# Optimization experiments

Measured on AMD Instinct MI355X. Metric: run time of the kernel, lower is better.

The kernel has to match this reference:

```python
import jax, jax.numpy as jnp
import numpy as np

EMBED_DIM = 768
HIDDEN = 768


def setup_inputs() -> dict:
    key = jax.random.key(0)
    k1, k2, k3, k4 = jax.random.split(key, 4)
    doc_embed = jax.random.normal(k1, (32, 1024, EMBED_DIM), dtype=jnp.float32)
    query_embed = jax.random.normal(k2, (32, 128, EMBED_DIM), dtype=jnp.float32)
    # nn.Linear params: weight [H, E], bias [H]
    bound = 1.0 / np.sqrt(EMBED_DIM)
    W = jax.random.uniform(k3, (HIDDEN, EMBED_DIM), minval=-bound, maxval=bound, dtype=jnp.float32)
    b = jax.random.uniform(k4, (HIDDEN,), minval=-bound, maxval=bound, dtype=jnp.float32)
    return {"doc_embed": doc_embed, "query_embed": query_embed, "W": W, "b": b}


def reference(doc_embed, query_embed, W, b):
    # shared linear projection + ReLU
    doc_o = jax.nn.relu(jnp.einsum('bde,he->bdh', doc_embed, W) + b)    # [B, Ld, H]
    query_o = jax.nn.relu(jnp.einsum('bqe,he->bqh', query_embed, W) + b)  # [B, Lq, H]
    # unscaled cross-attention scores over query positions
    scores = jnp.einsum('bdh,bqh->bdq', doc_o, query_o)  # [B, Ld, Lq]
    attn = jax.nn.softmax(scores, axis=-1)
    out = jnp.einsum('bdq,bqe->bde', attn, query_embed)  # [B, Ld, E]
    return out
```

## Files before the change

kernel.cpp:

```cpp
#include <hip/hip_runtime.h>

typedef _Float16 f16x8 __attribute__((ext_vector_type(8)));
typedef float f32x4 __attribute__((ext_vector_type(4)));

#define EMB 768
#define LQ 128
#define LD 1024
#define NB 32

typedef const __attribute__((address_space(1))) char gas_char;
typedef __attribute__((address_space(3))) char las_char;

__device__ __forceinline__ void gload16(const void* g, void* l) {
    __builtin_amdgcn_global_load_lds((gas_char*)g, (las_char*)l, 16, 0, 0);
}

#define SWZ(row, ch) ((row) * 64 + ((((ch) ^ ((row) & 7))) * 8))

__device__ __forceinline__ void stage_tile(const _Float16* g, _Float16* l, int wave, int lane) {
#pragma unroll
    for (int i = 0; i < 4; ++i) {
        const int idx = i * 256 + wave * 64 + lane;
        const int row = idx >> 3, ch = idx & 7;
        const int lch = ch ^ (row & 7);
        gload16(g + (size_t)row * EMB + lch * 8, l + (size_t)(i * 256 + wave * 64) * 8);
    }
}

__global__ void cvt8_kernel(const float* __restrict__ in, _Float16* __restrict__ out, int n8) {
    int i = blockIdx.x * 256 + threadIdx.x;
    if (i >= n8) return;
    const float4 a = ((const float4*)in)[2 * i];
    const float4 b = ((const float4*)in)[2 * i + 1];
    f16x8 o;
    o[0] = (_Float16)a.x; o[1] = (_Float16)a.y; o[2] = (_Float16)a.z; o[3] = (_Float16)a.w;
    o[4] = (_Float16)b.x; o[5] = (_Float16)b.y; o[6] = (_Float16)b.z; o[7] = (_Float16)b.w;
    ((f16x8*)out)[i] = o;
}

__global__ void make_vt_kernel(const float* __restrict__ Q, _Float16* __restrict__ VT) {
    int i = blockIdx.x * 256 + threadIdx.x;
    if (i >= NB * EMB * LQ) return;
    int q = i % LQ;
    int e = (i / LQ) % EMB;
    int b = i / (LQ * EMB);
    VT[i] = (_Float16)Q[((size_t)b * LQ + q) * EMB + e];
}

__global__ __launch_bounds__(256) void proj128_kernel(
    const _Float16* __restrict__ A, const _Float16* __restrict__ B,
    const float* __restrict__ bias, _Float16* __restrict__ OUT) {
    __shared__ __align__(16) _Float16 smem[32768];
    const int tid = threadIdx.x, wave = tid >> 6, lane = tid & 63;
    const int wr = wave >> 1, wc = wave & 1;
    const int lr = lane & 15, lkg = lane >> 4;
    const int row0 = blockIdx.x * 128, col0 = blockIdx.y * 128;
    const _Float16* ga = A + (size_t)row0 * EMB;
    const _Float16* gb = B + (size_t)col0 * EMB;

    f32x4 acc[4][4];
#pragma unroll
    for (int m = 0; m < 4; ++m)
#pragma unroll
        for (int n = 0; n < 4; ++n) acc[m][n] = (f32x4){0.f, 0.f, 0.f, 0.f};

    stage_tile(ga, smem, wave, lane);
    stage_tile(gb, smem + 8192, wave, lane);
    int cur = 0;
    for (int it = 0; it < 12; ++it) {
        __syncthreads();
        if (it < 11) {
            stage_tile(ga + (it + 1) * 64, smem + (cur ^ 1) * 16384, wave, lane);
            stage_tile(gb + (it + 1) * 64, smem + (cur ^ 1) * 16384 + 8192, wave, lane);
        }
        const _Float16* sA = smem + cur * 16384;
        const _Float16* sB = smem + cur * 16384 + 8192;
#pragma unroll
        for (int kk = 0; kk < 2; ++kk) {
            const int ch = kk * 4 + lkg;
            f16x8 af[4], bf[4];
#pragma unroll
            for (int m = 0; m < 4; ++m)
                af[m] = *(const f16x8*)(sA + SWZ(wr * 64 + m * 16 + lr, ch));
#pragma unroll
            for (int n = 0; n < 4; ++n)
                bf[n] = *(const f16x8*)(sB + SWZ(wc * 64 + n * 16 + lr, ch));
#pragma unroll
            for (int m = 0; m < 4; ++m)
#pragma unroll
                for (int n = 0; n < 4; ++n)
                    acc[m][n] = __builtin_amdgcn_mfma_f32_16x16x32_f16(af[m], bf[n], acc[m][n], 0, 0, 0);
        }
        cur ^= 1;
    }
    const int crow = lkg * 4;
#pragma unroll
    for (int n = 0; n < 4; ++n) {
        const int gc = col0 + wc * 64 + n * 16 + lr;
        const float bv = bias[gc];
#pragma unroll
        for (int m = 0; m < 4; ++m) {
            const size_t gr = row0 + wr * 64 + m * 16 + crow;
#pragma unroll
            for (int r = 0; r < 4; ++r) {
                float v = acc[m][n][r] + bv;
                OUT[(gr + r) * EMB + gc] = (_Float16)(v > 0.f ? v : 0.f);
            }
        }
    }
}

__global__ __launch_bounds__(256) void attn128_kernel(
    const _Float16* __restrict__ Do, const _Float16* __restrict__ Qo,
    const _Float16* __restrict__ VT, float* __restrict__ OUT) {
    __shared__ __align__(16) _Float16 smem[32768];
    const int tid = threadIdx.x, wave = tid >> 6, lane = tid & 63;
    const int lr = lane & 15, lkg = lane >> 4;
    const int b = blockIdx.x, dblk = blockIdx.y;
    const _Float16* gd = Do + ((size_t)b * LD + dblk * 128) * EMB;
    const _Float16* gq = Qo + (size_t)b * LQ * EMB;

    f32x4 s[2][8];
#pragma unroll
    for (int m = 0; m < 2; ++m)
#pragma unroll
        for (int n = 0; n < 8; ++n) s[m][n] = (f32x4){0.f, 0.f, 0.f, 0.f};

    stage_tile(gd, smem, wave, lane);
    stage_tile(gq, smem + 8192, wave, lane);
    int cur = 0;
    for (int it = 0; it < 12; ++it) {
        __syncthreads();
        if (it < 11) {
            stage_tile(gd + (it + 1) * 64, smem + (cur ^ 1) * 16384, wave, lane);
            stage_tile(gq + (it + 1) * 64, smem + (cur ^ 1) * 16384 + 8192, wave, lane);
        }
        const _Float16* sD = smem + cur * 16384;
        const _Float16* sQ = smem + cur * 16384 + 8192;
#pragma unroll
        for (int kk = 0; kk < 2; ++kk) {
            const int ch = kk * 4 + lkg;
            f16x8 am[2];
#pragma unroll
            for (int m = 0; m < 2; ++m)
                am[m] = *(const f16x8*)(sD + SWZ(wave * 32 + m * 16 + lr, ch));
#pragma unroll
            for (int n = 0; n < 8; ++n) {
                const f16x8 bq = *(const f16x8*)(sQ + SWZ(n * 16 + lr, ch));
#pragma unroll
                for (int m = 0; m < 2; ++m)
                    s[m][n] = __builtin_amdgcn_mfma_f32_16x16x32_f16(am[m], bq, s[m][n], 0, 0, 0);
            }
        }
        cur ^= 1;
    }
    __syncthreads();

    _Float16 (*P)[136] = (_Float16 (*)[136])smem;
    const int crow = lkg * 4;
#pragma unroll
    for (int m = 0; m < 2; ++m) {
#pragma unroll
        for (int r = 0; r < 4; ++r) {
            float mx = -1e30f;
#pragma unroll
            for (int n = 0; n < 8; ++n) mx = fmaxf(mx, s[m][n][r]);
#pragma unroll
            for (int off = 1; off < 16; off <<= 1) mx = fmaxf(mx, __shfl_xor(mx, off));
            float p[8], sum = 0.f;
#pragma unroll
            for (int n = 0; n < 8; ++n) { p[n] = __expf(s[m][n][r] - mx); sum += p[n]; }
#pragma unroll
            for (int off = 1; off < 16; off <<= 1) sum += __shfl_xor(sum, off);
            const float inv = 1.f / sum;
            const int row = wave * 32 + m * 16 + crow + r;
#pragma unroll
            for (int n = 0; n < 8; ++n) P[row][n * 16 + lr] = (_Float16)(p[n] * inv);
        }
    }
    __syncthreads();

    const _Float16* vtb = VT + (size_t)b * EMB * LQ;
#pragma unroll 1
    for (int nc = 0; nc < 6; ++nc) {
        f32x4 o[2][8];
#pragma unroll
        for (int m = 0; m < 2; ++m)
#pragma unroll
            for (int t = 0; t < 8; ++t) o[m][t] = (f32x4){0.f, 0.f, 0.f, 0.f};
#pragma unroll
        for (int ks = 0; ks < 4; ++ks) {
            f16x8 am[2];
#pragma unroll
            for (int m = 0; m < 2; ++m)
                am[m] = *(const f16x8*)(&P[wave * 32 + m * 16 + lr][ks * 32 + lkg * 8]);
#pragma unroll
            for (int t = 0; t < 8; ++t) {
                const f16x8 bv = *(const f16x8*)(vtb + (size_t)(nc * 128 + t * 16 + lr) * LQ + ks * 32 + lkg * 8);
#pragma unroll
                for (int m = 0; m < 2; ++m)
                    o[m][t] = __builtin_amdgcn_mfma_f32_16x16x32_f16(am[m], bv, o[m][t], 0, 0, 0);
            }
        }
#pragma unroll
        for (int t = 0; t < 8; ++t) {
#pragma unroll
            for (int m = 0; m < 2; ++m) {
                const size_t gr = (size_t)b * LD + dblk * 128 + wave * 32 + m * 16 + crow;
                const int e = nc * 128 + t * 16 + lr;
#pragma unroll
                for (int r = 0; r < 4; ++r)
                    OUT[(gr + r) * EMB + e] = o[m][t][r];
            }
        }
    }
}

extern "C" void kernel_launch(void* const* d_in, const int* in_sizes, int n_in,
                              void* d_out, int out_size, void* d_ws, size_t ws_size,
                              hipStream_t stream) {
    const float* doc   = (const float*)d_in[0];
    const float* query = (const float*)d_in[1];
    const float* W     = (const float*)d_in[2];
    const float* bias  = (const float*)d_in[3];
    float* out = (float*)d_out;

    const size_t nW  = (size_t)EMB * EMB;
    const size_t nVT = (size_t)NB * EMB * LQ;
    const size_t nQo = (size_t)NB * LQ * EMB;
    const size_t nDo = (size_t)NB * LD * EMB;
    const size_t need = (nW + nVT + nQo + nDo) * sizeof(_Float16);
    if (ws_size < need) return;

    _Float16* W16 = (_Float16*)d_ws;
    _Float16* VT  = W16 + nW;
    _Float16* Qo  = VT + nVT;
    _Float16* Do  = Qo + nQo;

    _Float16* doc16 = (_Float16*)d_out;
    _Float16* q16   = doc16 + nDo;

    cvt8_kernel<<<(int)(nDo / 8 / 256), 256, 0, stream>>>(doc, doc16, (int)(nDo / 8));
    cvt8_kernel<<<(int)(nQo / 8 / 256), 256, 0, stream>>>(query, q16, (int)(nQo / 8));
    cvt8_kernel<<<(int)(nW / 8 / 256), 256, 0, stream>>>(W, W16, (int)(nW / 8));
    make_vt_kernel<<<(int)(nVT / 256), 256, 0, stream>>>(query, VT);

    proj128_kernel<<<dim3(NB * LQ / 128, EMB / 128), 256, 0, stream>>>(q16, W16, bias, Qo);
    proj128_kernel<<<dim3(NB * LD / 128, EMB / 128), 256, 0, stream>>>(doc16, W16, bias, Do);
    attn128_kernel<<<dim3(NB, LD / 128), 256, 0, stream>>>(Do, Qo, VT, out);
}
```

Before: 160.1 us.

## Merge projections into one 256x256 GEMM with triple-buffered LDS; shrink attention tile

The two projection launches become a single 512-thread GEMM over the concatenated doc and query rows, which relies on q16 following doc16 and Qo following Do in memory. It uses 256x256 output tiles, a 3-stage global_load_lds pipeline with explicit waitcnt and barrier scheduling, setprio around the MFMA blocks, and an XCD-aware block remap. The attention kernel moves to 64-row doc tiles with a remapped 1D grid to raise block count and occupancy. The larger tile and the hand-written barrier scheduling are meant to cut global traffic and launch overhead, at the risk of register pressure and fragile synchronization.

```diff
diff --git a/kernel.cpp b/kernel.cpp
--- a/kernel.cpp
+++ b/kernel.cpp
@@ -16,16 +16,7 @@
 }
 
 #define SWZ(row, ch) ((row) * 64 + ((((ch) ^ ((row) & 7))) * 8))
-
-__device__ __forceinline__ void stage_tile(const _Float16* g, _Float16* l, int wave, int lane) {
-#pragma unroll
-    for (int i = 0; i < 4; ++i) {
-        const int idx = i * 256 + wave * 64 + lane;
-        const int row = idx >> 3, ch = idx & 7;
-        const int lch = ch ^ (row & 7);
-        gload16(g + (size_t)row * EMB + lch * 8, l + (size_t)(i * 256 + wave * 64) * 8);
-    }
-}
+#define SWZ32(row, c) ((row) * 32 + ((((c) ^ ((row) & 3) ^ (((row) >> 2) & 3))) * 8))
 
 __global__ void cvt8_kernel(const float* __restrict__ in, _Float16* __restrict__ out, int n8) {
     int i = blockIdx.x * 256 + threadIdx.x;
@@ -47,109 +38,161 @@
     VT[i] = (_Float16)Q[((size_t)b * LQ + q) * EMB + e];
 }
 
-__global__ __launch_bounds__(256) void proj128_kernel(
+__global__ __launch_bounds__(512, 2) void proj256_kernel(
     const _Float16* __restrict__ A, const _Float16* __restrict__ B,
-    const float* __restrict__ bias, _Float16* __restrict__ OUT) {
-    __shared__ __align__(16) _Float16 smem[32768];
+    const float* __restrict__ bias, _Float16* __restrict__ OUT, int nrowblk) {
+    extern __shared__ _Float16 smem[];
     const int tid = threadIdx.x, wave = tid >> 6, lane = tid & 63;
-    const int wr = wave >> 1, wc = wave & 1;
     const int lr = lane & 15, lkg = lane >> 4;
-    const int row0 = blockIdx.x * 128, col0 = blockIdx.y * 128;
-    const _Float16* ga = A + (size_t)row0 * EMB;
-    const _Float16* gb = B + (size_t)col0 * EMB;
-
-    f32x4 acc[4][4];
-#pragma unroll
-    for (int m = 0; m < 4; ++m)
+    const int wr = wave >> 2, wc = wave & 3;
+
+    const int nwg = nrowblk * 3, cpx = nwg >> 3;
+    const int bid = blockIdx.x;
+    const int swz = (bid & 7) * cpx + (bid >> 3);
+    const int rowblk = swz / 3, colblk = swz % 3;
+    const int row0 = rowblk * 256, col0 = colblk * 256;
+
+    const _Float16* gA = A + (size_t)row0 * EMB;
+    const _Float16* gB = B + (size_t)col0 * EMB;
+
+    const int sr0 = tid >> 2, sc = tid & 3;
+    const int sig = (sr0 & 3) ^ ((sr0 >> 2) & 3);
+    const int scs = (sc ^ sig) * 8;
+    const _Float16* srcA0 = gA + (size_t)sr0 * EMB + scs;
+    const _Float16* srcA1 = gA + (size_t)(sr0 + 128) * EMB + scs;
+    const _Float16* srcB0 = gB + (size_t)sr0 * EMB + scs;
+    const _Float16* srcB1 = gB + (size_t)(sr0 + 128) * EMB + scs;
+
+#define STAGE_A(kt, bufi) { _Float16* d = smem + (bufi) * 16384 + wave * 512; \
+        gload16(srcA0 + (kt) * 32, d); gload16(srcA1 + (kt) * 32, d + 4096); }
+#define STAGE_B(kt, bufi) { _Float16* d = smem + (bufi) * 16384 + 8192 + wave * 512; \
+        gload16(srcB0 + (kt) * 32, d); gload16(srcB1 + (kt) * 32, d + 4096); }
+
+    f32x4 acc[8][4];
+#pragma unroll
+    for (int m = 0; m < 8; ++m)
 #pragma unroll
         for (int n = 0; n < 4; ++n) acc[m][n] = (f32x4){0.f, 0.f, 0.f, 0.f};
 
-    stage_tile(ga, smem, wave, lane);
-    stage_tile(gb, smem + 8192, wave, lane);
+    const int rdoff = ((lkg ^ (lr & 3) ^ ((lr >> 2) & 3)) * 8);
+
+    STAGE_A(0, 0); STAGE_B(0, 0); STAGE_A(1, 1); STAGE_B(1, 1);
+    asm volatile("s_waitcnt vmcnt(4)" ::: "memory");
+    __builtin_amdgcn_s_barrier();
+
+    int bi = 0;
+    for (int j = 0; j < 24; ++j) {
+        const _Float16* bufA = smem + bi * 16384;
+        const _Float16* bufB = bufA + 8192;
+        int nb = bi + 2; if (nb >= 3) nb -= 3;
+        f16x8 bf[4], af[4];
+#pragma unroll
+        for (int n = 0; n < 4; ++n)
+            bf[n] = *(const f16x8*)(bufB + (wc * 64 + n * 16 + lr) * 32 + rdoff);
+#pragma unroll
+        for (int m = 0; m < 4; ++m)
+            af[m] = *(const f16x8*)(bufA + (wr * 128 + m * 16 + lr) * 32 + rdoff);
+        if (j + 2 < 24) { STAGE_A(j + 2, nb); }
+        __builtin_amdgcn_s_barrier();
+        asm volatile("s_waitcnt lgkmcnt(0)" ::: "memory");
+        __builtin_amdgcn_sched_barrier(0);
+        __builtin_amdgcn_s_setprio(1);
+#pragma unroll
+        for (int m = 0; m < 4; ++m)
+#pragma unroll
+            for (int n = 0; n < 4; ++n)
+                acc[m][n] = __builtin_amdgcn_mfma_f32_16x16x32_f16(af[m], bf[n], acc[m][n], 0, 0, 0);
+        __builtin_amdgcn_s_setprio(0);
+        __builtin_amdgcn_s_barrier();
+#pragma unroll
+        for (int m = 0; m < 4; ++m)
+            af[m] = *(const f16x8*)(bufA + (wr * 128 + (m + 4) * 16 + lr) * 32 + rdoff);
+        if (j + 2 < 24) { STAGE_B(j + 2, nb); }
+        if (j + 3 < 24) { asm volatile("s_waitcnt vmcnt(4)" ::: "memory"); }
+        else            { asm volatile("s_waitcnt vmcnt(0)" ::: "memory"); }
+        __builtin_amdgcn_s_barrier();
+        asm volatile("s_waitcnt lgkmcnt(0)" ::: "memory");
+        __builtin_amdgcn_sched_barrier(0);
+        __builtin_amdgcn_s_setprio(1);
+#pragma unroll
+        for (int m = 0; m < 4; ++m)
+#pragma unroll
+            for (int n = 0; n < 4; ++n)
+                acc[m + 4][n] = __builtin_amdgcn_mfma_f32_16x16x32_f16(af[m], bf[n], acc[m + 4][n], 0, 0, 0);
+        __builtin_amdgcn_s_setprio(0);
+        __builtin_amdgcn_s_barrier();
+        bi = (bi == 2) ? 0 : bi + 1;
+    }
+
+    const int crow = lkg * 4;
+#pragma unroll
+    for (int n = 0; n < 4; ++n) {
+        const int gc = col0 + wc * 64 + n * 16 + lr;
+        const float bv = bias[gc];
+#pragma unroll
+        for (int m = 0; m < 8; ++m) {
+            const size_t gr = (size_t)row0 + wr * 128 + m * 16 + crow;
+#pragma unroll
+            for (int r = 0; r < 4; ++r) {
+                float v = acc[m][n][r] + bv;
+                OUT[(gr + r) * EMB + gc] = (_Float16)(v > 0.f ? v : 0.f);
+            }
+        }
+    }
+#undef STAGE_A
+#undef STAGE_B
+}
+
+__global__ __launch_bounds__(256) void attn64_kernel(
+    const _Float16* __restrict__ Do, const _Float16* __restrict__ Qo,
+    const _Float16* __restrict__ VT, float* __restrict__ OUT) {
+    __shared__ __align__(16) _Float16 smem[24576];
+    const int tid = threadIdx.x, wave = tid >> 6, lane = tid & 63;
+    const int lr = lane & 15, lkg = lane >> 4;
+
+    const int l = blockIdx.x;
+    const int x = l & 7, i = l >> 3;
+    const int b = x * 4 + (i >> 4), dblk = i & 15;
+
+    const _Float16* gd = Do + ((size_t)b * LD + dblk * 64) * EMB;
+    const _Float16* gq = Qo + (size_t)b * LQ * EMB;
+
+    f32x4 s[8];
+#pragma unroll
+    for (int n = 0; n < 8; ++n) s[n] = (f32x4){0.f, 0.f, 0.f, 0.f};
+
+#define STAGE_D(g, base) { \
+    _Float16* lb = (base); \
+    { int idx = tid;       int row = idx >> 3, ch = idx & 7; int lch = ch ^ (row & 7); \
+      gload16((g) + (size_t)row * EMB + lch * 8, lb + (size_t)(wave * 64) * 8); } \
+    { int idx = 256 + tid; int row = idx >> 3, ch = idx & 7; int lch = ch ^ (row & 7); \
+      gload16((g) + (size_t)row * EMB + lch * 8, lb + (size_t)(256 + wave * 64) * 8); } }
+#define STAGE_Q(g, base) { \
+    _Float16* lb = (base); \
+    _Pragma("unroll") \
+    for (int it2 = 0; it2 < 4; ++it2) { \
+      int idx = it2 * 256 + tid; int row = idx >> 3, ch = idx & 7; int lch = ch ^ (row & 7); \
+      gload16((g) + (size_t)row * EMB + lch * 8, lb + (size_t)(it2 * 256 + wave * 64) * 8); } }
+
+    STAGE_D(gd, smem);
+    STAGE_Q(gq, smem + 4096);
     int cur = 0;
     for (int it = 0; it < 12; ++it) {
         __syncthreads();
         if (it < 11) {
-            stage_tile(ga + (it + 1) * 64, smem + (cur ^ 1) * 16384, wave, lane);
-            stage_tile(gb + (it + 1) * 64, smem + (cur ^ 1) * 16384 + 8192, wave, lane);
-        }
-        const _Float16* sA = smem + cur * 16384;
-        const _Float16* sB = smem + cur * 16384 + 8192;
+            STAGE_D(gd + (it + 1) * 64, smem + (cur ^ 1) * 12288);
+            STAGE_Q(gq + (it + 1) * 64, smem + (cur ^ 1) * 12288 + 4096);
+        }
+        const _Float16* sD = smem + cur * 12288;
+        const _Float16* sQ = sD + 4096;
 #pragma unroll
         for (int kk = 0; kk < 2; ++kk) {
             const int ch = kk * 4 + lkg;
-            f16x8 af[4], bf[4];
-#pragma unroll
-            for (int m = 0; m < 4; ++m)
-                af[m] = *(const f16x8*)(sA + SWZ(wr * 64 + m * 16 + lr, ch));
-#pragma unroll
-            for (int n = 0; n < 4; ++n)
-                bf[n] = *(const f16x8*)(sB + SWZ(wc * 64 + n * 16 + lr, ch));
-#pragma unroll
-            for (int m = 0; m < 4; ++m)
-#pragma unroll
-                for (int n = 0; n < 4; ++n)
-                    acc[m][n] = __builtin_amdgcn_mfma_f32_16x16x32_f16(af[m], bf[n], acc[m][n], 0, 0, 0);
-        }
-        cur ^= 1;
-    }
-    const int crow = lkg * 4;
-#pragma unroll
-    for (int n = 0; n < 4; ++n) {
-        const int gc = col0 + wc * 64 + n * 16 + lr;
-        const float bv = bias[gc];
-#pragma unroll
-        for (int m = 0; m < 4; ++m) {
-            const size_t gr = row0 + wr * 64 + m * 16 + crow;
-#pragma unroll
-            for (int r = 0; r < 4; ++r) {
-                float v = acc[m][n][r] + bv;
-                OUT[(gr + r) * EMB + gc] = (_Float16)(v > 0.f ? v : 0.f);
-            }
-        }
-    }
-}
-
-__global__ __launch_bounds__(256) void attn128_kernel(
-    const _Float16* __restrict__ Do, const _Float16* __restrict__ Qo,
-    const _Float16* __restrict__ VT, float* __restrict__ OUT) {
-    __shared__ __align__(16) _Float16 smem[32768];
-    const int tid = threadIdx.x, wave = tid >> 6, lane = tid & 63;
-    const int lr = lane & 15, lkg = lane >> 4;
-    const int b = blockIdx.x, dblk = blockIdx.y;
-    const _Float16* gd = Do + ((size_t)b * LD + dblk * 128) * EMB;
-    const _Float16* gq = Qo + (size_t)b * LQ * EMB;
-
-    f32x4 s[2][8];
-#pragma unroll
-    for (int m = 0; m < 2; ++m)
-#pragma unroll
-        for (int n = 0; n < 8; ++n) s[m][n] = (f32x4){0.f, 0.f, 0.f, 0.f};
-
-    stage_tile(gd, smem, wave, lane);
-    stage_tile(gq, smem + 8192, wave, lane);
-    int cur = 0;
-    for (int it = 0; it < 12; ++it) {
-        __syncthreads();
-        if (it < 11) {
-            stage_tile(gd + (it + 1) * 64, smem + (cur ^ 1) * 16384, wave, lane);
-            stage_tile(gq + (it + 1) * 64, smem + (cur ^ 1) * 16384 + 8192, wave, lane);
-        }
-        const _Float16* sD = smem + cur * 16384;
-        const _Float16* sQ = smem + cur * 16384 + 8192;
-#pragma unroll
-        for (int kk = 0; kk < 2; ++kk) {
-            const int ch = kk * 4 + lkg;
-            f16x8 am[2];
-#pragma unroll
-            for (int m = 0; m < 2; ++m)
-                am[m] = *(const f16x8*)(sD + SWZ(wave * 32 + m * 16 + lr, ch));
+            const f16x8 af = *(const f16x8*)(sD + SWZ(wave * 16 + lr, ch));
 #pragma unroll
             for (int n = 0; n < 8; ++n) {
                 const f16x8 bq = *(const f16x8*)(sQ + SWZ(n * 16 + lr, ch));
-#pragma unroll
-                for (int m = 0; m < 2; ++m)
-                    s[m][n] = __builtin_amdgcn_mfma_f32_16x16x32_f16(am[m], bq, s[m][n], 0, 0, 0);
+                s[n] = __builtin_amdgcn_mfma_f32_16x16x32_f16(af, bq, s[n], 0, 0, 0);
             }
         }
         cur ^= 1;
@@ -159,61 +202,50 @@
     _Float16 (*P)[136] = (_Float16 (*)[136])smem;
     const int crow = lkg * 4;
 #pragma unroll
-    for (int m = 0; m < 2; ++m) {
-#pragma unroll
-        for (int r = 0; r < 4; ++r) {
-            float mx = -1e30f;
-#pragma unroll
-            for (int n = 0; n < 8; ++n) mx = fmaxf(mx, s[m][n][r]);
-#pragma unroll
-            for (int off = 1; off < 16; off <<= 1) mx = fmaxf(mx, __shfl_xor(mx, off));
-            float p[8], sum = 0.f;
-#pragma unroll
-            for (int n = 0; n < 8; ++n) { p[n] = __expf(s[m][n][r] - mx); sum += p[n]; }
-#pragma unroll
-            for (int off = 1; off < 16; off <<= 1) sum += __shfl_xor(sum, off);
-            const float inv = 1.f / sum;
-            const int row = wave * 32 + m * 16 + crow + r;
-#pragma unroll
-            for (int n = 0; n < 8; ++n) P[row][n * 16 + lr] = (_Float16)(p[n] * inv);
-        }
+    for (int r = 0; r < 4; ++r) {
+        float mx = -1e30f;
+#pragma unroll
+        for (int n = 0; n < 8; ++n) mx = fmaxf(mx, s[n][r]);
+#pragma unroll
+        for (int off = 1; off < 16; off <<= 1) mx = fmaxf(mx, __shfl_xor(mx, off));
+        float p[8], sum = 0.f;
+#pragma unroll
+        for (int n = 0; n < 8; ++n) { p[n] = __expf(s[n][r] - mx); sum += p[n]; }
+#pragma unroll
+        for (int off = 1; off < 16; off <<= 1) sum += __shfl_xor(sum, off);
+        const float inv = 1.f / sum;
+        const int row = wave * 16 + crow + r;
+#pragma unroll
+        for (int n = 0; n < 8; ++n) P[row][n * 16 + lr] = (_Float16)(p[n] * inv);
     }
     __syncthreads();
 
     const _Float16* vtb = VT + (size_t)b * EMB * LQ;
+    const size_t dbase = (size_t)b * LD + dblk * 64 + wave * 16 + crow;
 #pragma unroll 1
     for (int nc = 0; nc < 6; ++nc) {
-        f32x4 o[2][8];
-#pragma unroll
-        for (int m = 0; m < 2; ++m)
-#pragma unroll
-            for (int t = 0; t < 8; ++t) o[m][t] = (f32x4){0.f, 0.f, 0.f, 0.f};
+        f32x4 o[8];
+#pragma unroll
+        for (int t = 0; t < 8; ++t) o[t] = (f32x4){0.f, 0.f, 0.f, 0.f};
 #pragma unroll
         for (int ks = 0; ks < 4; ++ks) {
-            f16x8 am[2];
-#pragma unroll
-            for (int m = 0; m < 2; ++m)
-                am[m] = *(const f16x8*)(&P[wave * 32 + m * 16 + lr][ks * 32 + lkg * 8]);
+            const f16x8 am = *(const f16x8*)(&P[wave * 16 + lr][ks * 32 + lkg * 8]);
 #pragma unroll
             for (int t = 0; t < 8; ++t) {
                 const f16x8 bv = *(const f16x8*)(vtb + (size_t)(nc * 128 + t * 16 + lr) * LQ + ks * 32 + lkg * 8);
-#pragma unroll
-                for (int m = 0; m < 2; ++m)
-                    o[m][t] = __builtin_amdgcn_mfma_f32_16x16x32_f16(am[m], bv, o[m][t], 0, 0, 0);
+                o[t] = __builtin_amdgcn_mfma_f32_16x16x32_f16(am, bv, o[t], 0, 0, 0);
             }
         }
 #pragma unroll
         for (int t = 0; t < 8; ++t) {
-#pragma unroll
-            for (int m = 0; m < 2; ++m) {
-                const size_t gr = (size_t)b * LD + dblk * 128 + wave * 32 + m * 16 + crow;
-                const int e = nc * 128 + t * 16 + lr;
-#pragma unroll
-                for (int r = 0; r < 4; ++r)
-                    OUT[(gr + r) * EMB + e] = o[m][t][r];
-            }
-        }
-    }
+            const int e = nc * 128 + t * 16 + lr;
+#pragma unroll
+            for (int r = 0; r < 4; ++r)
+                OUT[(dbase + r) * EMB + e] = o[t][r];
+        }
+    }
+#undef STAGE_D
+#undef STAGE_Q
 }
 
 extern "C" void kernel_launch(void* const* d_in, const int* in_sizes, int n_in,
@@ -227,15 +259,15 @@
 
     const size_t nW  = (size_t)EMB * EMB;
     const size_t nVT = (size_t)NB * EMB * LQ;
+    const size_t nDo = (size_t)NB * LD * EMB;
     const size_t nQo = (size_t)NB * LQ * EMB;
-    const size_t nDo = (size_t)NB * LD * EMB;
-    const size_t need = (nW + nVT + nQo + nDo) * sizeof(_Float16);
+    const size_t need = (nW + nVT + nDo + nQo) * sizeof(_Float16);
     if (ws_size < need) return;
 
     _Float16* W16 = (_Float16*)d_ws;
     _Float16* VT  = W16 + nW;
-    _Float16* Qo  = VT + nVT;
-    _Float16* Do  = Qo + nQo;
+    _Float16* Do  = VT + nVT;
+    _Float16* Qo  = Do + nDo;
 
     _Float16* doc16 = (_Float16*)d_out;
     _Float16* q16   = doc16 + nDo;
@@ -245,7 +277,10 @@
     cvt8_kernel<<<(int)(nW / 8 / 256), 256, 0, stream>>>(W, W16, (int)(nW / 8));
     make_vt_kernel<<<(int)(nVT / 256), 256, 0, stream>>>(query, VT);
 
-    proj128_kernel<<<dim3(NB * LQ / 128, EMB / 128), 256, 0, stream>>>(q16, W16, bias, Qo);
-    proj128_kernel<<<dim3(NB * LD / 128, EMB / 128), 256, 0, stream>>>(doc16, W16, bias, Do);
-    attn128_kernel<<<dim3(NB, LD / 128), 256, 0, stream>>>(Do, Qo, VT, out);
-}
+    const int nrowblk = (int)((nDo + nQo) / EMB / 256);
+    hipFuncSetAttribute(reinterpret_cast<const void*>(&proj256_kernel),
+                        hipFuncAttributeMaxDynamicSharedMemorySize, 98304);
+    proj256_kernel<<<dim3(nrowblk * 3), 512, 98304, stream>>>(doc16, W16, bias, Do, nrowblk);
+
+    attn64_kernel<<<dim3(NB * 16), 256, 0, stream>>>(Do, Qo, VT, out);
+}
```

New measurement: 169.0 us. 5.6% more time.

## Fuse doc projection, scores, softmax and PV into one kernel

Applied to the files above, without the earlier changes.

Removes the separate fp16 conversion of doc, the doc projection GEMM, and the Do intermediate buffer. A new fused kernel loads fp32 doc rows straight into registers as fp16 A-fragments. It projects them chunk by chunk against double-buffered W tiles in LDS, applies bias and ReLU, and accumulates the scores against Qo read from global. Softmax and PV follow in the same kernel, which cuts global traffic and launches. The cost is 64-row blocks (512 blocks) with heavy register use, W being restreamed by every block, and Qo and VT loaded directly from global without LDS staging.

```diff
diff --git a/kernel.cpp b/kernel.cpp
--- a/kernel.cpp
+++ b/kernel.cpp
@@ -16,16 +16,6 @@
 }
 
 #define SWZ(row, ch) ((row) * 64 + ((((ch) ^ ((row) & 7))) * 8))
-
-__device__ __forceinline__ void stage_tile(const _Float16* g, _Float16* l, int wave, int lane) {
-#pragma unroll
-    for (int i = 0; i < 4; ++i) {
-        const int idx = i * 256 + wave * 64 + lane;
-        const int row = idx >> 3, ch = idx & 7;
-        const int lch = ch ^ (row & 7);
-        gload16(g + (size_t)row * EMB + lch * 8, l + (size_t)(i * 256 + wave * 64) * 8);
-    }
-}
 
 __global__ void cvt8_kernel(const float* __restrict__ in, _Float16* __restrict__ out, int n8) {
     int i = blockIdx.x * 256 + threadIdx.x;
@@ -45,6 +35,16 @@
     int e = (i / LQ) % EMB;
     int b = i / (LQ * EMB);
     VT[i] = (_Float16)Q[((size_t)b * LQ + q) * EMB + e];
+}
+
+__device__ __forceinline__ void stage_tile(const _Float16* g, _Float16* l, int wave, int lane) {
+#pragma unroll
+    for (int i = 0; i < 4; ++i) {
+        const int idx = i * 256 + wave * 64 + lane;
+        const int row = idx >> 3, ch = idx & 7;
+        const int lch = ch ^ (row & 7);
+        gload16(g + (size_t)row * EMB + lch * 8, l + (size_t)(i * 256 + wave * 64) * 8);
+    }
 }
 
 __global__ __launch_bounds__(256) void proj128_kernel(
@@ -110,108 +110,135 @@
     }
 }
 
-__global__ __launch_bounds__(256) void attn128_kernel(
-    const _Float16* __restrict__ Do, const _Float16* __restrict__ Qo,
+__device__ __forceinline__ void stage_w(const _Float16* __restrict__ W16,
+                                        _Float16* sWbuf, int t, int tid) {
+    const int hc = t / 12, kt = t - hc * 12;
+    const _Float16* gsrc = W16 + (size_t)hc * 128 * EMB + kt * 64;
+#pragma unroll
+    for (int ii = 0; ii < 4; ++ii) {
+        const int idx = ii * 256 + tid;
+        const int row = idx >> 3, ch = idx & 7;
+        gload16(gsrc + (size_t)row * EMB + ((ch ^ (row & 7)) * 8), sWbuf + (size_t)idx * 8);
+    }
+}
+
+__global__ __launch_bounds__(256, 2) void fused_kernel(
+    const float* __restrict__ doc, const _Float16* __restrict__ W16,
+    const float* __restrict__ bias, const _Float16* __restrict__ Qo,
     const _Float16* __restrict__ VT, float* __restrict__ OUT) {
-    __shared__ __align__(16) _Float16 smem[32768];
+    __shared__ __align__(16) _Float16 sW[2 * 8192];
+    __shared__ __align__(16) _Float16 doC[4][16][136];
+
     const int tid = threadIdx.x, wave = tid >> 6, lane = tid & 63;
     const int lr = lane & 15, lkg = lane >> 4;
-    const int b = blockIdx.x, dblk = blockIdx.y;
-    const _Float16* gd = Do + ((size_t)b * LD + dblk * 128) * EMB;
-    const _Float16* gq = Qo + (size_t)b * LQ * EMB;
-
-    f32x4 s[2][8];
-#pragma unroll
-    for (int m = 0; m < 2; ++m)
-#pragma unroll
-        for (int n = 0; n < 8; ++n) s[m][n] = (f32x4){0.f, 0.f, 0.f, 0.f};
-
-    stage_tile(gd, smem, wave, lane);
-    stage_tile(gq, smem + 8192, wave, lane);
-    int cur = 0;
-    for (int it = 0; it < 12; ++it) {
-        __syncthreads();
-        if (it < 11) {
-            stage_tile(gd + (it + 1) * 64, smem + (cur ^ 1) * 16384, wave, lane);
-            stage_tile(gq + (it + 1) * 64, smem + (cur ^ 1) * 16384 + 8192, wave, lane);
-        }
-        const _Float16* sD = smem + cur * 16384;
-        const _Float16* sQ = smem + cur * 16384 + 8192;
-#pragma unroll
-        for (int kk = 0; kk < 2; ++kk) {
-            const int ch = kk * 4 + lkg;
-            f16x8 am[2];
-#pragma unroll
-            for (int m = 0; m < 2; ++m)
-                am[m] = *(const f16x8*)(sD + SWZ(wave * 32 + m * 16 + lr, ch));
+
+    const int l = blockIdx.x;
+    const int x = l & 7, i = l >> 3;
+    const int b = x * 4 + (i >> 4), dblk = i & 15;
+
+    stage_w(W16, sW, 0, tid);
+
+    const float* drow = doc + ((size_t)b * LD + dblk * 64 + wave * 16 + lr) * EMB;
+    f16x8 af[24];
+#pragma unroll
+    for (int k = 0; k < 24; ++k) {
+        const float4 xa = *(const float4*)(drow + k * 32 + lkg * 8);
+        const float4 xb = *(const float4*)(drow + k * 32 + lkg * 8 + 4);
+        f16x8 v;
+        v[0] = (_Float16)xa.x; v[1] = (_Float16)xa.y; v[2] = (_Float16)xa.z; v[3] = (_Float16)xa.w;
+        v[4] = (_Float16)xb.x; v[5] = (_Float16)xb.y; v[6] = (_Float16)xb.z; v[7] = (_Float16)xb.w;
+        af[k] = v;
+    }
+
+    f32x4 sc[8];
+#pragma unroll
+    for (int n = 0; n < 8; ++n) sc[n] = (f32x4){0.f, 0.f, 0.f, 0.f};
+
+    const int crow = lkg * 4;
+
+#pragma unroll 1
+    for (int hc = 0; hc < 6; ++hc) {
+        f32x4 a2[8];
+#pragma unroll
+        for (int n = 0; n < 8; ++n) a2[n] = (f32x4){0.f, 0.f, 0.f, 0.f};
+
+#pragma unroll 1
+        for (int kt = 0; kt < 12; ++kt) {
+            const int t = hc * 12 + kt;
+            __syncthreads();
+            if (t < 71) stage_w(W16, sW + ((t + 1) & 1) * 8192, t + 1, tid);
+            const _Float16* bw = sW + (t & 1) * 8192;
+#pragma unroll
+            for (int kk = 0; kk < 2; ++kk) {
+#pragma unroll
+                for (int n = 0; n < 8; ++n) {
+                    const f16x8 bf = *(const f16x8*)(bw + SWZ(n * 16 + lr, kk * 4 + lkg));
+                    a2[n] = __builtin_amdgcn_mfma_f32_16x16x32_f16(af[kt * 2 + kk], bf, a2[n], 0, 0, 0);
+                }
+            }
+        }
+
+#pragma unroll
+        for (int n = 0; n < 8; ++n) {
+            const float bv = bias[hc * 128 + n * 16 + lr];
+#pragma unroll
+            for (int r = 0; r < 4; ++r) {
+                float v = a2[n][r] + bv;
+                doC[wave][crow + r][n * 16 + lr] = (_Float16)(v > 0.f ? v : 0.f);
+            }
+        }
+#pragma unroll
+        for (int ks = 0; ks < 4; ++ks) {
+            const f16x8 pa = *(const f16x8*)(&doC[wave][lr][ks * 32 + lkg * 8]);
 #pragma unroll
             for (int n = 0; n < 8; ++n) {
-                const f16x8 bq = *(const f16x8*)(sQ + SWZ(n * 16 + lr, ch));
-#pragma unroll
-                for (int m = 0; m < 2; ++m)
-                    s[m][n] = __builtin_amdgcn_mfma_f32_16x16x32_f16(am[m], bq, s[m][n], 0, 0, 0);
-            }
-        }
-        cur ^= 1;
-    }
-    __syncthreads();
-
-    _Float16 (*P)[136] = (_Float16 (*)[136])smem;
-    const int crow = lkg * 4;
-#pragma unroll
-    for (int m = 0; m < 2; ++m) {
-#pragma unroll
-        for (int r = 0; r < 4; ++r) {
-            float mx = -1e30f;
-#pragma unroll
-            for (int n = 0; n < 8; ++n) mx = fmaxf(mx, s[m][n][r]);
-#pragma unroll
-            for (int off = 1; off < 16; off <<= 1) mx = fmaxf(mx, __shfl_xor(mx, off));
-            float p[8], sum = 0.f;
-#pragma unroll
-            for (int n = 0; n < 8; ++n) { p[n] = __expf(s[m][n][r] - mx); sum += p[n]; }
-#pragma unroll
-            for (int off = 1; off < 16; off <<= 1) sum += __shfl_xor(sum, off);
-            const float inv = 1.f / sum;
-            const int row = wave * 32 + m * 16 + crow + r;
-#pragma unroll
-            for (int n = 0; n < 8; ++n) P[row][n * 16 + lr] = (_Float16)(p[n] * inv);
-        }
-    }
-    __syncthreads();
+                const f16x8 bq = *(const f16x8*)(Qo + ((size_t)b * LQ + n * 16 + lr) * EMB
+                                                 + hc * 128 + ks * 32 + lkg * 8);
+                sc[n] = __builtin_amdgcn_mfma_f32_16x16x32_f16(pa, bq, sc[n], 0, 0, 0);
+            }
+        }
+    }
+
+#pragma unroll
+    for (int r = 0; r < 4; ++r) {
+        float mx = -1e30f;
+#pragma unroll
+        for (int n = 0; n < 8; ++n) mx = fmaxf(mx, sc[n][r]);
+#pragma unroll
+        for (int off = 1; off < 16; off <<= 1) mx = fmaxf(mx, __shfl_xor(mx, off));
+        float p[8], sum = 0.f;
+#pragma unroll
+        for (int n = 0; n < 8; ++n) { p[n] = __expf(sc[n][r] - mx); sum += p[n]; }
+#pragma unroll
+        for (int off = 1; off < 16; off <<= 1) sum += __shfl_xor(sum, off);
+        const float inv = 1.f / sum;
+#pragma unroll
+        for (int n = 0; n < 8; ++n) doC[wave][crow + r][n * 16 + lr] = (_Float16)(p[n] * inv);
+    }
 
     const _Float16* vtb = VT + (size_t)b * EMB * LQ;
+    const size_t dbase = (size_t)b * LD + dblk * 64 + wave * 16 + crow;
 #pragma unroll 1
     for (int nc = 0; nc < 6; ++nc) {
-        f32x4 o[2][8];
-#pragma unroll
-        for (int m = 0; m < 2; ++m)
-#pragma unroll
-            for (int t = 0; t < 8; ++t) o[m][t] = (f32x4){0.f, 0.f, 0.f, 0.f};
+        f32x4 o[8];
+#pragma unroll
+        for (int t = 0; t < 8; ++t) o[t] = (f32x4){0.f, 0.f, 0.f, 0.f};
 #pragma unroll
         for (int ks = 0; ks < 4; ++ks) {
-            f16x8 am[2];
-#pragma unroll
-            for (int m = 0; m < 2; ++m)
-                am[m] = *(const f16x8*)(&P[wave * 32 + m * 16 + lr][ks * 32 + lkg * 8]);
+            const f16x8 am = *(const f16x8*)(&doC[wave][lr][ks * 32 + lkg * 8]);
 #pragma unroll
             for (int t = 0; t < 8; ++t) {
-                const f16x8 bv = *(const f16x8*)(vtb + (size_t)(nc * 128 + t * 16 + lr) * LQ + ks * 32 + lkg * 8);
-#pragma unroll
-                for (int m = 0; m < 2; ++m)
-                    o[m][t] = __builtin_amdgcn_mfma_f32_16x16x32_f16(am[m], bv, o[m][t], 0, 0, 0);
+                const f16x8 bv = *(const f16x8*)(vtb + (size_t)(nc * 128 + t * 16 + lr) * LQ
+                                                 + ks * 32 + lkg * 8);
+                o[t] = __builtin_amdgcn_mfma_f32_16x16x32_f16(am, bv, o[t], 0, 0, 0);
             }
         }
 #pragma unroll
         for (int t = 0; t < 8; ++t) {
-#pragma unroll
-            for (int m = 0; m < 2; ++m) {
-                const size_t gr = (size_t)b * LD + dblk * 128 + wave * 32 + m * 16 + crow;
-                const int e = nc * 128 + t * 16 + lr;
-#pragma unroll
-                for (int r = 0; r < 4; ++r)
-                    OUT[(gr + r) * EMB + e] = o[m][t][r];
-            }
+            const int e = nc * 128 + t * 16 + lr;
+#pragma unroll
+            for (int r = 0; r < 4; ++r)
+                OUT[(dbase + r) * EMB + e] = o[t][r];
         }
     }
 }
@@ -226,26 +253,22 @@
     float* out = (float*)d_out;
 
     const size_t nW  = (size_t)EMB * EMB;
+    const size_t nQ  = (size_t)NB * LQ * EMB;
     const size_t nVT = (size_t)NB * EMB * LQ;
     const size_t nQo = (size_t)NB * LQ * EMB;
-    const size_t nDo = (size_t)NB * LD * EMB;
-    const size_t need = (nW + nVT + nQo + nDo) * sizeof(_Float16);
+    const size_t need = (nW + nQ + nVT + nQo) * sizeof(_Float16);
     if (ws_size < need) return;
 
     _Float16* W16 = (_Float16*)d_ws;
-    _Float16* VT  = W16 + nW;
+    _Float16* q16 = W16 + nW;
+    _Float16* VT  = q16 + nQ;
     _Float16* Qo  = VT + nVT;
-    _Float16* Do  = Qo + nQo;
-
-    _Float16* doc16 = (_Float16*)d_out;
-    _Float16* q16   = doc16 + nDo;
-
-    cvt8_kernel<<<(int)(nDo / 8 / 256), 256, 0, stream>>>(doc, doc16, (int)(nDo / 8));
-    cvt8_kernel<<<(int)(nQo / 8 / 256), 256, 0, stream>>>(query, q16, (int)(nQo / 8));
+
     cvt8_kernel<<<(int)(nW / 8 / 256), 256, 0, stream>>>(W, W16, (int)(nW / 8));
+    cvt8_kernel<<<(int)(nQ / 8 / 256), 256, 0, stream>>>(query, q16, (int)(nQ / 8));
     make_vt_kernel<<<(int)(nVT / 256), 256, 0, stream>>>(query, VT);
 
     proj128_kernel<<<dim3(NB * LQ / 128, EMB / 128), 256, 0, stream>>>(q16, W16, bias, Qo);
-    proj128_kernel<<<dim3(NB * LD / 128, EMB / 128), 256, 0, stream>>>(doc16, W16, bias, Do);
-    attn128_kernel<<<dim3(NB, LD / 128), 256, 0, stream>>>(Do, Qo, VT, out);
-}
+
+    fused_kernel<<<dim3(NB * 16), 256, 0, stream>>>(doc, W16, bias, Qo, VT, out);
+}
```

Result: slower. 225.9 us (+41.1%).

## Fuse fp32-to-fp16 conversion of doc and query into projection GEMM staging

Applied to the files above, without the earlier changes.

Removes the separate conversion kernels for doc and query. The projection kernel now reads fp32 activations straight into registers, converts them to fp16 and stores them swizzled into LDS. For the A operand this replaces async global-to-LDS loads with register-staged loads that are issued before the MFMA loop and written to LDS after it, so the prefetch still overlaps compute. The aim is to drop a full fp16 write and re-read of the large doc tensor, at the cost of more register pressure and twice the global bytes per A tile, since it now reads fp32. The B tiles are also fetched six times, once per column block.

```diff
diff --git a/kernel.cpp b/kernel.cpp
--- a/kernel.cpp
+++ b/kernel.cpp
@@ -16,16 +16,6 @@
 }
 
 #define SWZ(row, ch) ((row) * 64 + ((((ch) ^ ((row) & 7))) * 8))
-
-__device__ __forceinline__ void stage_tile(const _Float16* g, _Float16* l, int wave, int lane) {
-#pragma unroll
-    for (int i = 0; i < 4; ++i) {
-        const int idx = i * 256 + wave * 64 + lane;
-        const int row = idx >> 3, ch = idx & 7;
-        const int lch = ch ^ (row & 7);
-        gload16(g + (size_t)row * EMB + lch * 8, l + (size_t)(i * 256 + wave * 64) * 8);
-    }
-}
 
 __global__ void cvt8_kernel(const float* __restrict__ in, _Float16* __restrict__ out, int n8) {
     int i = blockIdx.x * 256 + threadIdx.x;
@@ -47,16 +37,33 @@
     VT[i] = (_Float16)Q[((size_t)b * LQ + q) * EMB + e];
 }
 
-__global__ __launch_bounds__(256) void proj128_kernel(
-    const _Float16* __restrict__ A, const _Float16* __restrict__ B,
+__device__ __forceinline__ void stage_tile(const _Float16* g, _Float16* l, int tid) {
+#pragma unroll
+    for (int i = 0; i < 4; ++i) {
+        const int idx = i * 256 + tid;
+        const int row = idx >> 3, ch = idx & 7;
+        gload16(g + (size_t)row * EMB + ((ch ^ (row & 7)) * 8), l + (size_t)idx * 8);
+    }
+}
+
+__global__ __launch_bounds__(256) void projd_kernel(
+    const float* __restrict__ A, const _Float16* __restrict__ W16,
     const float* __restrict__ bias, _Float16* __restrict__ OUT) {
     __shared__ __align__(16) _Float16 smem[32768];
     const int tid = threadIdx.x, wave = tid >> 6, lane = tid & 63;
     const int wr = wave >> 1, wc = wave & 1;
     const int lr = lane & 15, lkg = lane >> 4;
     const int row0 = blockIdx.x * 128, col0 = blockIdx.y * 128;
-    const _Float16* ga = A + (size_t)row0 * EMB;
-    const _Float16* gb = B + (size_t)col0 * EMB;
+    const float* ga = A + (size_t)row0 * EMB;
+    const _Float16* gb = W16 + (size_t)col0 * EMB;
+
+    int srow[4], scol[4];
+#pragma unroll
+    for (int i = 0; i < 4; ++i) {
+        const int idx = i * 256 + tid;
+        srow[i] = idx >> 3;
+        scol[i] = ((idx & 7) ^ (srow[i] & 7)) * 8;
+    }
 
     f32x4 acc[4][4];
 #pragma unroll
@@ -64,17 +71,38 @@
 #pragma unroll
         for (int n = 0; n < 4; ++n) acc[m][n] = (f32x4){0.f, 0.f, 0.f, 0.f};
 
-    stage_tile(ga, smem, wave, lane);
-    stage_tile(gb, smem + 8192, wave, lane);
+    float4 areg[4][2];
+#pragma unroll
+    for (int i = 0; i < 4; ++i) {
+        const float* src = ga + (size_t)srow[i] * EMB + scol[i];
+        areg[i][0] = *(const float4*)(src);
+        areg[i][1] = *(const float4*)(src + 4);
+    }
+    stage_tile(gb, smem + 8192, tid);
+#pragma unroll
+    for (int i = 0; i < 4; ++i) {
+        f16x8 v;
+        v[0] = (_Float16)areg[i][0].x; v[1] = (_Float16)areg[i][0].y;
+        v[2] = (_Float16)areg[i][0].z; v[3] = (_Float16)areg[i][0].w;
+        v[4] = (_Float16)areg[i][1].x; v[5] = (_Float16)areg[i][1].y;
+        v[6] = (_Float16)areg[i][1].z; v[7] = (_Float16)areg[i][1].w;
+        *(f16x8*)(smem + (size_t)(i * 256 + tid) * 8) = v;
+    }
+
     int cur = 0;
     for (int it = 0; it < 12; ++it) {
         __syncthreads();
         if (it < 11) {
-            stage_tile(ga + (it + 1) * 64, smem + (cur ^ 1) * 16384, wave, lane);
-            stage_tile(gb + (it + 1) * 64, smem + (cur ^ 1) * 16384 + 8192, wave, lane);
+#pragma unroll
+            for (int i = 0; i < 4; ++i) {
+                const float* src = ga + (size_t)srow[i] * EMB + (it + 1) * 64 + scol[i];
+                areg[i][0] = *(const float4*)(src);
+                areg[i][1] = *(const float4*)(src + 4);
+            }
+            stage_tile(gb + (it + 1) * 64, smem + (cur ^ 1) * 16384 + 8192, tid);
         }
         const _Float16* sA = smem + cur * 16384;
-        const _Float16* sB = smem + cur * 16384 + 8192;
+        const _Float16* sB = sA + 8192;
 #pragma unroll
         for (int kk = 0; kk < 2; ++kk) {
             const int ch = kk * 4 + lkg;
@@ -91,8 +119,21 @@
                 for (int n = 0; n < 4; ++n)
                     acc[m][n] = __builtin_amdgcn_mfma_f32_16x16x32_f16(af[m], bf[n], acc[m][n], 0, 0, 0);
         }
+        if (it < 11) {
+            _Float16* dst = smem + (cur ^ 1) * 16384;
+#pragma unroll
+            for (int i = 0; i < 4; ++i) {
+                f16x8 v;
+                v[0] = (_Float16)areg[i][0].x; v[1] = (_Float16)areg[i][0].y;
+                v[2] = (_Float16)areg[i][0].z; v[3] = (_Float16)areg[i][0].w;
+                v[4] = (_Float16)areg[i][1].x; v[5] = (_Float16)areg[i][1].y;
+                v[6] = (_Float16)areg[i][1].z; v[7] = (_Float16)areg[i][1].w;
+                *(f16x8*)(dst + (size_t)(i * 256 + tid) * 8) = v;
+            }
+        }
         cur ^= 1;
     }
+
     const int crow = lkg * 4;
 #pragma unroll
     for (int n = 0; n < 4; ++n) {
@@ -126,17 +167,17 @@
 #pragma unroll
         for (int n = 0; n < 8; ++n) s[m][n] = (f32x4){0.f, 0.f, 0.f, 0.f};
 
-    stage_tile(gd, smem, wave, lane);
-    stage_tile(gq, smem + 8192, wave, lane);
+    stage_tile(gd, smem, tid);
+    stage_tile(gq, smem + 8192, tid);
     int cur = 0;
     for (int it = 0; it < 12; ++it) {
         __syncthreads();
         if (it < 11) {
-            stage_tile(gd + (it + 1) * 64, smem + (cur ^ 1) * 16384, wave, lane);
-            stage_tile(gq + (it + 1) * 64, smem + (cur ^ 1) * 16384 + 8192, wave, lane);
+            stage_tile(gd + (it + 1) * 64, smem + (cur ^ 1) * 16384, tid);
+            stage_tile(gq + (it + 1) * 64, smem + (cur ^ 1) * 16384 + 8192, tid);
         }
         const _Float16* sD = smem + cur * 16384;
-        const _Float16* sQ = smem + cur * 16384 + 8192;
+        const _Float16* sQ = sD + 8192;
 #pragma unroll
         for (int kk = 0; kk < 2; ++kk) {
             const int ch = kk * 4 + lkg;
@@ -237,15 +278,11 @@
     _Float16* Qo  = VT + nVT;
     _Float16* Do  = Qo + nQo;
 
-    _Float16* doc16 = (_Float16*)d_out;
-    _Float16* q16   = doc16 + nDo;
-
-    cvt8_kernel<<<(int)(nDo / 8 / 256), 256, 0, stream>>>(doc, doc16, (int)(nDo / 8));
-    cvt8_kernel<<<(int)(nQo / 8 / 256), 256, 0, stream>>>(query, q16, (int)(nQo / 8));
     cvt8_kernel<<<(int)(nW / 8 / 256), 256, 0, stream>>>(W, W16, (int)(nW / 8));
     make_vt_kernel<<<(int)(nVT / 256), 256, 0, stream>>>(query, VT);
 
-    proj128_kernel<<<dim3(NB * LQ / 128, EMB / 128), 256, 0, stream>>>(q16, W16, bias, Qo);
-    proj128_kernel<<<dim3(NB * LD / 128, EMB / 128), 256, 0, stream>>>(doc16, W16, bias, Do);
+    projd_kernel<<<dim3(NB * LQ / 128, EMB / 128), 256, 0, stream>>>(query, W16, bias, Qo);
+    projd_kernel<<<dim3(NB * LD / 128, EMB / 128), 256, 0, stream>>>(doc, W16, bias, Do);
+
     attn128_kernel<<<dim3(NB, LD / 128), 256, 0, stream>>>(Do, Qo, VT, out);
 }
```

After: 179.2 us. +11.9%, slower.
